# Performance work log

Hardware: AMD Instinct MI355X
Metric: run time of the kernel (lower is better)

Reference implementation:

```python
import jax, jax.numpy as jnp
import numpy as np

B, H, N, D = 4, 8, 256, 32

def setup_inputs() -> dict:
    key = jax.random.key(0)
    k1, k2, k3, k4 = jax.random.split(key, 4)
    q = jax.random.normal(k1, (B, H, N, D), dtype=jnp.float32)
    k = jax.random.normal(k2, (B, H, N, D), dtype=jnp.float32)
    v = jax.random.normal(k3, (B, H, N, D), dtype=jnp.float32)
    edges_feats = jax.random.normal(k4, (B, H, N, N, D), dtype=jnp.float32)
    mask = jnp.zeros((B, N, N), dtype=jnp.float32)
    return {"q": q, "k": k, "v": v, "edges_feats": edges_feats, "mask": mask}

def reference(q, k, v, edges_feats, mask):
    b, h, n, d = q.shape
    # edge-modulated scores: [B,H,n,n,d]
    scores = q[:, :, :, None, :] * k[:, :, None, :, :] * edges_feats
    logits = scores.sum(axis=-1) / jnp.sqrt(jnp.float32(d))  # [B,H,n,n]
    logits = logits + mask[:, None, :, :]
    attn = jax.nn.softmax(logits, axis=3)
    out = jnp.einsum('bhij,bhjd->bhid', attn, v)              # [B,H,n,d]
    out = jnp.transpose(out, (0, 2, 1, 3)).reshape(b, n, h * d)
    # scores.transpose(1,3): [B,H,n,n,d] -> [B,n,n,H,d] -> [B,n,n,H*d]
    edge_out = jnp.transpose(scores, (0, 3, 2, 1, 4)).reshape(b, n, n, h * d)
    return out, edge_out
```

## Files before the change

### kernel.cpp

```cpp
#include <hip/hip_runtime.h>
#include <math.h>

constexpr int B = 4, H = 8, N = 256, D = 32;
constexpr int HD = H * D;

typedef float nfloat4 __attribute__((ext_vector_type(4)));

__global__ __launch_bounds__(256) void fused_edge_attn(
    const float* __restrict__ q,
    const float* __restrict__ k,
    const float* __restrict__ v,
    const float* __restrict__ E,
    const float* __restrict__ mask,
    float* __restrict__ out,
    float* __restrict__ edge_out)
{
    const int tid = threadIdx.x;
    const int blk = blockIdx.x;
    const int i = blk % N;
    const int h = (blk / N) % H;
    const int b = blk / (N * H);

    __shared__ float logits[N];
    __shared__ float red[256];
    __shared__ float wred[4];
    __shared__ float wsum[4];

    const size_t bh = (size_t)(b * H + h);
    const nfloat4* __restrict__ E4 = (const nfloat4*)(E + (bh * N + (size_t)i) * (size_t)(N * D));
    const nfloat4* __restrict__ K4 = (const nfloat4*)(k + bh * (size_t)(N * D));
    const float*   qrow = q + (bh * N + (size_t)i) * D;

    const int d4 = tid & 7;
    const int jq = tid >> 3;
    const nfloat4 q4 = ((const nfloat4*)qrow)[d4];

    nfloat4* __restrict__ eo_base = (nfloat4*)(edge_out + ((size_t)b * N * N + i) * HD + h * D) + d4;

    #pragma unroll
    for (int iter = 0; iter < 8; ++iter) {
        const int j = iter * 32 + jq;
        const nfloat4 e  = __builtin_nontemporal_load(E4 + j * 8 + d4);
        const nfloat4 kk = K4[j * 8 + d4];
        const nfloat4 s = q4 * kk * e;
        __builtin_nontemporal_store(s, eo_base + (size_t)j * (N * HD / 4));
        float partial = s.x + s.y + s.z + s.w;
        partial += __shfl_xor(partial, 1);
        partial += __shfl_xor(partial, 2);
        partial += __shfl_xor(partial, 4);
        if (d4 == 0) logits[j] = partial;
    }
    __syncthreads();

    const float scale = 0.17677669529663687f;
    const float l = logits[tid] * scale + mask[((size_t)b * N + i) * N + tid];
    const int lane = tid & 63, wid = tid >> 6;

    float m = l;
    #pragma unroll
    for (int off = 32; off > 0; off >>= 1) m = fmaxf(m, __shfl_xor(m, off));
    if (lane == 0) wred[wid] = m;
    __syncthreads();
    m = fmaxf(fmaxf(wred[0], wred[1]), fmaxf(wred[2], wred[3]));

    const float ex = __expf(l - m);
    float ssum = ex;
    #pragma unroll
    for (int off = 32; off > 0; off >>= 1) ssum += __shfl_xor(ssum, off);
    if (lane == 0) wsum[wid] = ssum;
    __syncthreads();
    const float denom = wsum[0] + wsum[1] + wsum[2] + wsum[3];
    logits[tid] = ex / denom;
    __syncthreads();

    const float* vrow = v + bh * (size_t)(N * D);
    const int d = tid & 31;
    const int g = tid >> 5;
    float acc = 0.f;
    #pragma unroll
    for (int jj = 0; jj < 32; ++jj) {
        const int j = jj * 8 + g;
        acc += logits[j] * vrow[j * D + d];
    }
    red[tid] = acc;
    __syncthreads();
    if (tid < 32) {
        float o = red[tid] + red[32 + tid] + red[64 + tid] + red[96 + tid]
                + red[128 + tid] + red[160 + tid] + red[192 + tid] + red[224 + tid];
        out[(((size_t)b * N + i) * HD) + h * D + tid] = o;
    }
}

extern "C" void kernel_launch(void* const* d_in, const int* in_sizes, int n_in,
                              void* d_out, int out_size, void* d_ws, size_t ws_size,
                              hipStream_t stream) {
    const float* q    = (const float*)d_in[0];
    const float* k    = (const float*)d_in[1];
    const float* v    = (const float*)d_in[2];
    const float* E    = (const float*)d_in[3];
    const float* mask = (const float*)d_in[4];

    float* out      = (float*)d_out;
    float* edge_out = out + (size_t)B * N * HD;

    fused_edge_attn<<<B * H * N, 256, 0, stream>>>(q, k, v, E, mask, out, edge_out);
}
```

Measured before the change: 445.4 us.

## Split into edge-score kernel with shared-memory transpose and softmax-PV kernel

The fused kernel is split in two. The first kernel handles all 8 heads for a 32-column j tile and stages the scores in shared memory, so each edge_out row of H*D contiguous floats is written as one full 1 KB segment instead of 128-byte fragments scattered across heads. Logits go to a workspace buffer, and a second kernel does the softmax and the PV product. This trades an extra logits round trip (about 8 MB) and a second launch for better-coalesced stores on the dominant 67 MB edge_out write, and it falls back to the fused kernel when the workspace is too small.

New measurement: 473.4 us. +6.3%, slower.

```diff
diff --git a/kernel.cpp b/kernel.cpp
--- a/kernel.cpp
+++ b/kernel.cpp
@@ -5,6 +5,122 @@
 constexpr int HD = H * D;
 
 typedef float nfloat4 __attribute__((ext_vector_type(4)));
+
+__global__ __launch_bounds__(256) void edge_scores(
+    const float* __restrict__ q,
+    const float* __restrict__ k,
+    const float* __restrict__ E,
+    float* __restrict__ edge_out,
+    float* __restrict__ logits_ws)
+{
+    const int tid = threadIdx.x;
+    const int blk = blockIdx.x;
+    const int i  = blk % N;
+    const int jt = (blk / N) & 7;
+    const int b  = blk / (N * 8);
+    const int j0 = jt * 32;
+
+    __shared__ float sm[32][260];
+    __shared__ float lgsm[8][32];
+
+    const int d4 = tid & 7;
+    const int jl = tid >> 3;
+
+    #pragma unroll
+    for (int h = 0; h < 8; ++h) {
+        const size_t bh = (size_t)(b * H + h);
+        const nfloat4* E4 = (const nfloat4*)(E + (((bh * N + (size_t)i) * N) + j0) * (size_t)D);
+        const nfloat4* K4 = (const nfloat4*)(k + (bh * N + (size_t)j0) * (size_t)D);
+        const nfloat4  q4 = ((const nfloat4*)(q + (bh * N + (size_t)i) * (size_t)D))[d4];
+
+        const nfloat4 e  = __builtin_nontemporal_load(E4 + tid);
+        const nfloat4 kk = K4[jl * 8 + d4];
+        const nfloat4 s  = q4 * kk * e;
+
+        *(nfloat4*)&sm[jl][h * 32 + d4 * 4] = s;
+
+        float p = s.x + s.y + s.z + s.w;
+        p += __shfl_xor(p, 1);
+        p += __shfl_xor(p, 2);
+        p += __shfl_xor(p, 4);
+        if (d4 == 0) lgsm[h][jl] = p;
+    }
+    __syncthreads();
+
+    {
+        const int h = tid >> 5, jl2 = tid & 31;
+        logits_ws[(((size_t)(b * H + h) * N + i) * N) + j0 + jl2] = lgsm[h][jl2];
+    }
+
+    const int lane = tid & 63, wid = tid >> 6;
+    #pragma unroll
+    for (int r = 0; r < 8; ++r) {
+        const int jlr = wid * 8 + r;
+        const int j = j0 + jlr;
+        const nfloat4 val = *(const nfloat4*)&sm[jlr][lane * 4];
+        nfloat4* dst = (nfloat4*)(edge_out + (((size_t)b * N + j) * N + i) * (size_t)HD) + lane;
+        __builtin_nontemporal_store(val, dst);
+    }
+}
+
+__global__ __launch_bounds__(256) void softmax_pv(
+    const float* __restrict__ v,
+    const float* __restrict__ logits_ws,
+    const float* __restrict__ mask,
+    float* __restrict__ out)
+{
+    const int tid = threadIdx.x;
+    const int blk = blockIdx.x;
+    const int i = blk % N;
+    const int h = (blk / N) % H;
+    const int b = blk / (N * H);
+
+    __shared__ float probs[N];
+    __shared__ float red[256];
+    __shared__ float wred[4];
+    __shared__ float wsum[4];
+
+    const size_t bh = (size_t)(b * H + h);
+
+    const float scale = 0.17677669529663687f;
+    const float l = logits_ws[(bh * N + (size_t)i) * N + tid] * scale
+                  + mask[((size_t)b * N + i) * N + tid];
+    const int lane = tid & 63, wid = tid >> 6;
+
+    float m = l;
+    #pragma unroll
+    for (int off = 32; off > 0; off >>= 1) m = fmaxf(m, __shfl_xor(m, off));
+    if (lane == 0) wred[wid] = m;
+    __syncthreads();
+    m = fmaxf(fmaxf(wred[0], wred[1]), fmaxf(wred[2], wred[3]));
+
+    const float ex = __expf(l - m);
+    float ssum = ex;
+    #pragma unroll
+    for (int off = 32; off > 0; off >>= 1) ssum += __shfl_xor(ssum, off);
+    if (lane == 0) wsum[wid] = ssum;
+    __syncthreads();
+    const float denom = wsum[0] + wsum[1] + wsum[2] + wsum[3];
+    probs[tid] = ex / denom;
+    __syncthreads();
+
+    const float* vrow = v + bh * (size_t)(N * D);
+    const int d = tid & 31;
+    const int g = tid >> 5;
+    float acc = 0.f;
+    #pragma unroll
+    for (int jj = 0; jj < 32; ++jj) {
+        const int j = jj * 8 + g;
+        acc += probs[j] * vrow[j * D + d];
+    }
+    red[tid] = acc;
+    __syncthreads();
+    if (tid < 32) {
+        float o = red[tid] + red[32 + tid] + red[64 + tid] + red[96 + tid]
+                + red[128 + tid] + red[160 + tid] + red[192 + tid] + red[224 + tid];
+        out[(((size_t)b * N + i) * HD) + h * D + tid] = o;
+    }
+}
 
 __global__ __launch_bounds__(256) void fused_edge_attn(
     const float* __restrict__ q,
@@ -103,5 +219,12 @@
     float* out      = (float*)d_out;
     float* edge_out = out + (size_t)B * N * HD;
 
-    fused_edge_attn<<<B * H * N, 256, 0, stream>>>(q, k, v, E, mask, out, edge_out);
-}
+    const size_t logits_bytes = (size_t)B * H * N * N * sizeof(float);
+    if (ws_size >= logits_bytes) {
+        float* logits_ws = (float*)d_ws;
+        edge_scores<<<B * N * 8, 256, 0, stream>>>(q, k, E, edge_out, logits_ws);
+        softmax_pv<<<B * H * N, 256, 0, stream>>>(v, logits_ws, mask, out);
+    } else {
+        fused_edge_attn<<<B * H * N, 256, 0, stream>>>(q, k, v, E, mask, out, edge_out);
+    }
+}
```
